# Performance work log

Hardware: AMD Instinct MI355X
Metric: run time of the kernel (lower is better)

The kernel has to match this reference:

```python
import jax, jax.numpy as jnp
import numpy as np

B, T, C, H = 2, 2048, 1024, 16
HD = C // H  # head dim = 64


def setup_inputs() -> dict:
    key = jax.random.key(0)
    k1, k2, k3 = jax.random.split(key, 3)
    scale = 0.02
    x = jax.random.normal(k1, (B, T, C), dtype=jnp.float32)
    w_attn = jax.random.normal(k2, (C, 3 * C), dtype=jnp.float32) * scale
    b_attn = jnp.zeros((3 * C,), dtype=jnp.float32)
    w_proj = jax.random.normal(k3, (C, C), dtype=jnp.float32) * scale
    b_proj = jnp.zeros((C,), dtype=jnp.float32)
    return {"x": x, "w_attn": w_attn, "b_attn": b_attn, "w_proj": w_proj, "b_proj": b_proj}


def reference(x, w_attn, b_attn, w_proj, b_proj):
    b, t, c = x.shape
    qkv = x @ w_attn + b_attn  # [B,T,3C]
    q, k, v = jnp.split(qkv, 3, axis=-1)
    # [B,T,C] -> [B,H,T,HD]
    q = q.reshape(b, t, H, HD).transpose(0, 2, 1, 3)
    k = k.reshape(b, t, H, HD).transpose(0, 2, 1, 3)
    v = v.reshape(b, t, H, HD).transpose(0, 2, 1, 3)
    att = jnp.einsum('bhqd,bhkd->bhqk', q, k) * (1.0 / jnp.sqrt(jnp.float32(HD)))
    causal = jnp.tril(jnp.ones((t, t), dtype=bool))  # [T,T]
    att = jnp.where(causal[None, None, :, :], att, jnp.float32(-jnp.inf))
    att = jax.nn.softmax(att, axis=-1)
    y = jnp.einsum('bhqk,bhkd->bhqd', att, v)
    y = y.transpose(0, 2, 1, 3).reshape(b, t, c)
    return y @ w_proj + b_proj
```

## Files before the change

kernel.cpp:

```cpp
#include <hip/hip_runtime.h>


typedef unsigned short u16;
typedef unsigned short u16x8 __attribute__((ext_vector_type(8)));
typedef unsigned short u16x4 __attribute__((ext_vector_type(4)));
typedef __bf16 bf16x8 __attribute__((ext_vector_type(8)));
typedef __bf16 bf16x4 __attribute__((ext_vector_type(4)));
typedef float f32x4 __attribute__((ext_vector_type(4)));

#define MFMA16(a, b, c) __builtin_amdgcn_mfma_f32_16x16x32_bf16(a, b, c, 0, 0, 0)

static __device__ __forceinline__ u16 f2b(float f) {
  union { float f; unsigned int i; } x; x.f = f;
  unsigned int r = x.i + 0x7fffu + ((x.i >> 16) & 1u);
  return (u16)(r >> 16);
}
static __device__ __forceinline__ float b2f(u16 u) {
  union { unsigned int i; float f; } x; x.i = ((unsigned int)u) << 16; return x.f;
}

static __device__ __forceinline__ void gload_lds16(const u16* g, u16* l) {
#if defined(__HIP_DEVICE_COMPILE__)
  __builtin_amdgcn_global_load_lds(
      (const __attribute__((address_space(1))) unsigned int*)g,
      (__attribute__((address_space(3))) unsigned int*)l,
      16, 0, 0);
#else
  (void)g; (void)l;
#endif
}

__global__ __launch_bounds__(256) void cast_f32_bf16(
    const float* __restrict__ in, u16* __restrict__ out) {
  int i = (blockIdx.x * 256 + threadIdx.x) * 8;
  float4 a = *(const float4*)&in[i];
  float4 b = *(const float4*)&in[i + 4];
  u16x8 o;
  o[0] = f2b(a.x); o[1] = f2b(a.y); o[2] = f2b(a.z); o[3] = f2b(a.w);
  o[4] = f2b(b.x); o[5] = f2b(b.y); o[6] = f2b(b.z); o[7] = f2b(b.w);
  *(u16x8*)&out[i] = o;
}

__global__ __launch_bounds__(256) void transpose_f32_bf16(
    const float* __restrict__ in, u16* __restrict__ out, int R, int Cc) {
  __shared__ u16 tile[32][33];
  int bx = blockIdx.x, by = blockIdx.y;
  int tx = threadIdx.x, ty = threadIdx.y;
#pragma unroll
  for (int i = 0; i < 4; i++) {
    int r = by * 32 + ty + i * 8;
    int c = bx * 32 + tx;
    tile[ty + i * 8][tx] = f2b(in[r * Cc + c]);
  }
  __syncthreads();
#pragma unroll
  for (int i = 0; i < 4; i++) {
    int r = bx * 32 + ty + i * 8;
    int c = by * 32 + tx;
    out[r * R + c] = tile[tx][ty + i * 8];
  }
}

template <int MODE>
__global__ __launch_bounds__(256, 3) void gemm_bt(
    const u16* __restrict__ A, const u16* __restrict__ Bt,
    const float* __restrict__ bias, float* __restrict__ out,
    u16* __restrict__ Qb, u16* __restrict__ Kb, u16* __restrict__ Vtb,
    int M, int N, int K) {
  __shared__ u16 lA[128 * 32];
  __shared__ u16 lB[128 * 32];

  const int tid = threadIdx.x;
  const int lane = tid & 63;
  const int w = tid >> 6;
  const int wm = (w >> 1) * 64, wn = (w & 1) * 64;
  const int l15 = lane & 15, quad = lane >> 4;

  const int nx = gridDim.x;
  const int id = blockIdx.y * nx + blockIdx.x;
  const int chunk = (nx * gridDim.y) >> 3;
  const int nid = (id & 7) * chunk + (id >> 3);
  const int m0 = (nid / nx) * 128, n0 = (nid % nx) * 128;

  const bool swapcd = (MODE == 0) && (n0 < 2048);

  const int srow = lane >> 2;
  const int scol = (lane & 3) * 8;

  f32x4 acc[4][4] = {};

  for (int k0 = 0; k0 < K; k0 += 32) {
    __syncthreads();
#pragma unroll
    for (int h = 0; h < 2; h++) {
      int r = h * 64 + w * 16 + srow;
      gload_lds16(&A[(m0 + r) * K + k0 + scol], &lA[h * 2048 + w * 512 + lane * 8]);
      gload_lds16(&Bt[(n0 + r) * K + k0 + scol], &lB[h * 2048 + w * 512 + lane * 8]);
    }
    __syncthreads();

    bf16x8 af[4], bfr[4];
#pragma unroll
    for (int mi = 0; mi < 4; mi++)
      af[mi] = *(const bf16x8*)&lA[(wm + mi * 16 + l15) * 32 + quad * 8];
#pragma unroll
    for (int ni = 0; ni < 4; ni++)
      bfr[ni] = *(const bf16x8*)&lB[(wn + ni * 16 + l15) * 32 + quad * 8];
    if (swapcd) {
#pragma unroll
      for (int mi = 0; mi < 4; mi++)
#pragma unroll
        for (int ni = 0; ni < 4; ni++)
          acc[mi][ni] = MFMA16(bfr[ni], af[mi], acc[mi][ni]);
    } else {
#pragma unroll
      for (int mi = 0; mi < 4; mi++)
#pragma unroll
        for (int ni = 0; ni < 4; ni++)
          acc[mi][ni] = MFMA16(af[mi], bfr[ni], acc[mi][ni]);
    }
  }

  if (MODE == 1) {
#pragma unroll
    for (int mi = 0; mi < 4; mi++) {
#pragma unroll
      for (int ni = 0; ni < 4; ni++) {
        int n = n0 + wn + ni * 16 + l15;
        float bv = bias[n];
#pragma unroll
        for (int reg = 0; reg < 4; reg++) {
          int m = m0 + wm + mi * 16 + quad * 4 + reg;
          out[m * N + n] = acc[mi][ni][reg] + bv;
        }
      }
    }
  } else if (n0 < 2048) {
    const int which = n0 >> 10;
    u16* dst = which ? Kb : Qb;
    const float scale = which ? 0.18033688011112042f : 1.0f;
    const int b = m0 >> 11;
    const int hh = ((n0 & 1023) + wn) >> 6;
    const int tbase = (m0 & 2047) + wm + l15;
#pragma unroll
    for (int mi = 0; mi < 4; mi++) {
      u16* drow = dst + (((b << 4) + hh) * 2048 + tbase + mi * 16) * 64;
#pragma unroll
      for (int ni = 0; ni < 4; ni++) {
        int d0 = ni * 16 + quad * 4;
        float4 bv4 = *(const float4*)&bias[n0 + wn + d0];
        u16x4 o;
        o[0] = f2b((acc[mi][ni][0] + bv4.x) * scale);
        o[1] = f2b((acc[mi][ni][1] + bv4.y) * scale);
        o[2] = f2b((acc[mi][ni][2] + bv4.z) * scale);
        o[3] = f2b((acc[mi][ni][3] + bv4.w) * scale);
        *(u16x4*)&drow[d0] = o;
      }
    }
  } else {
    const int b = m0 >> 11;
    const int hh = ((n0 & 1023) + wn) >> 6;
    const int bh = (b << 4) + hh;
    const u16* unused = A; (void)unused;
#pragma unroll
    for (int mi = 0; mi < 4; mi++) {
      int t32 = (m0 & 2047) + wm + (mi >> 1) * 32;
      int tp0 = quad * 8 + (mi & 1) * 4;
#pragma unroll
      for (int ni = 0; ni < 4; ni++) {
        int d = ni * 16 + l15;
        float bv = bias[n0 + wn + d];
        u16x4 o;
        o[0] = f2b(acc[mi][ni][0] + bv);
        o[1] = f2b(acc[mi][ni][1] + bv);
        o[2] = f2b(acc[mi][ni][2] + bv);
        o[3] = f2b(acc[mi][ni][3] + bv);
        *(u16x4*)&Vtb[(bh * 64 + d) * 2048 + t32 + tp0] = o;
      }
    }
  }
}

__global__ __launch_bounds__(256, 4) void attn_split(
    const u16* __restrict__ Qg, const u16* __restrict__ Kg,
    const u16* __restrict__ Vt, u16* __restrict__ Yg,
    u16* __restrict__ Opart, float* __restrict__ lpart) {
  __shared__ u16 lk[2][64 * 64];
  __shared__ u16 lvt[2][64 * 64];

  const int x = blockIdx.x;
  const int bh = blockIdx.y;
  int qt, s, ns;
  if (x < 8)       { qt = x;                s = 0;            ns = 1; }
  else if (x < 24) { int r = x - 8;  qt = 8  + (r >> 1); s = r & 1; ns = 2; }
  else if (x < 48) { int r = x - 24; qt = 16 + r / 3;    s = r % 3; ns = 3; }
  else             { int r = x - 48; qt = 24 + (r >> 2); s = r & 3; ns = 4; }
  const int total = qt + 1;
  const int kts  = (s * total) / ns;
  const int kend = ((s + 1) * total) / ns;

  const int tid = threadIdx.x;
  const int lane = tid & 63;
  const int w = tid >> 6;
  const int l15 = lane & 15, quad = lane >> 4;
  const int qbase = qt * 64;
  const int base = bh * 2048 * 64;
  const int vbase = bh * 64 * 2048;
  const int qloc = w * 16 + l15;
  const int xsw = (l15 & 7) << 3;

  const int sr = tid >> 3;
  const int sc = (tid & 7) * 8;

  const u16* qrow = Qg + base + (qbase + w * 16 + l15) * 64;
  bf16x8 bq0 = *(const bf16x8*)&qrow[quad * 8];
  bf16x8 bq1 = *(const bf16x8*)&qrow[32 + quad * 8];

  u16x8 onesu = {0x3F80, 0x3F80, 0x3F80, 0x3F80, 0x3F80, 0x3F80, 0x3F80, 0x3F80};
  bf16x8 ones = *(const bf16x8*)&onesu;

  const u16* kp = Kg + base;
  const u16* vp = Vt + vbase;

  u16x8 kr[2], vr[2];
  {
    int kvb = kts * 64;
#pragma unroll
    for (int h = 0; h < 2; h++) {
      int r = sr + h * 32;
      kr[h] = *(const u16x8*)&kp[(kvb + r) * 64 + sc];
      vr[h] = *(const u16x8*)&vp[r * 2048 + kvb + sc];
    }
  }

  f32x4 oacc[4] = {};
  f32x4 lacc = {};

  int cur = 0;
  for (int kt = kts; kt < kend; kt++) {
    u16* lkc = lk[cur];
    u16* lvc = lvt[cur];
#pragma unroll
    for (int h = 0; h < 2; h++) {
      int r = sr + h * 32;
      int cs = sc ^ ((r & 7) << 3);
      *(u16x8*)&lkc[r * 64 + cs] = kr[h];
      *(u16x8*)&lvc[r * 64 + cs] = vr[h];
    }
    __syncthreads();
    if (kt + 1 < kend) {
      int kvb = (kt + 1) * 64;
#pragma unroll
      for (int h = 0; h < 2; h++) {
        int r = sr + h * 32;
        kr[h] = *(const u16x8*)&kp[(kvb + r) * 64 + sc];
        vr[h] = *(const u16x8*)&vp[r * 2048 + kvb + sc];
      }
    }

    const bool diag = (kt == qt);

#pragma unroll
    for (int u = 0; u < 2; u++) {
      bf16x8 pa;
#pragma unroll
      for (int half = 0; half < 2; half++) {
        int nt = 2 * u + half;
        const u16* kb = &lkc[(nt * 16 + l15) * 64];
        bf16x8 ak0 = *(const bf16x8*)&kb[(quad * 8) ^ xsw];
        bf16x8 ak1 = *(const bf16x8*)&kb[(32 + quad * 8) ^ xsw];
        f32x4 st = {};
        st = MFMA16(ak0, bq0, st);
        st = MFMA16(ak1, bq1, st);
#pragma unroll
        for (int reg = 0; reg < 4; reg++) {
          float sv = st[reg];
          if (diag && (nt * 16 + quad * 4 + reg) > qloc) sv = -1e30f;
          pa[half * 4 + reg] = (__bf16)__builtin_amdgcn_exp2f(sv);
        }
      }
      lacc = MFMA16(pa, ones, lacc);
#pragma unroll
      for (int dt = 0; dt < 4; dt++) {
        bf16x8 bv = *(const bf16x8*)&lvc[(dt * 16 + l15) * 64 +
                                         ((u * 32 + quad * 8) ^ xsw)];
        oacc[dt] = MFMA16(pa, bv, oacc[dt]);
      }
    }
    cur ^= 1;
  }

  if (ns == 1) {
    const int b = bh >> 4, hh = bh & 15;
    float inv[4];
#pragma unroll
    for (int reg = 0; reg < 4; reg++) inv[reg] = 1.0f / lacc[reg];
#pragma unroll
    for (int dt = 0; dt < 4; dt++)
#pragma unroll
      for (int reg = 0; reg < 4; reg++) {
        int q = qbase + w * 16 + quad * 4 + reg;
        int col = hh * 64 + dt * 16 + l15;
        Yg[(b * 2048 + q) * 1024 + col] = f2b(oacc[dt][reg] * inv[reg]);
      }
  } else {
    const int p = bh * 80 + x;
    u16* op = Opart + p * 4096 + (w * 16) * 64;
#pragma unroll
    for (int dt = 0; dt < 4; dt++)
#pragma unroll
      for (int reg = 0; reg < 4; reg++)
        op[(quad * 4 + reg) * 64 + dt * 16 + l15] = f2b(oacc[dt][reg]);
    if (l15 == 0) {
#pragma unroll
      for (int reg = 0; reg < 4; reg++)
        lpart[p * 64 + w * 16 + quad * 4 + reg] = lacc[reg];
    }
  }
}

__global__ __launch_bounds__(256) void attn_combine(
    const u16* __restrict__ Opart, const float* __restrict__ lpart,
    u16* __restrict__ Yg) {
  const int qt = 8 + blockIdx.x;
  const int bh = blockIdx.y;
  const int tid = threadIdx.x;
  const int row = tid >> 2;
  const int cg = (tid & 3) * 16;
  int xb, ns;
  if (qt < 16)      { xb = 8  + (qt - 8) * 2;  ns = 2; }
  else if (qt < 24) { xb = 24 + (qt - 16) * 3; ns = 3; }
  else              { xb = 48 + (qt - 24) * 4; ns = 4; }

  float acc[16] = {};
  float lsum = 0.f;
  for (int i = 0; i < ns; i++) {
    int p = bh * 80 + xb + i;
    lsum += lpart[p * 64 + row];
    const u16* oprow = Opart + p * 4096 + row * 64 + cg;
    u16x8 a = *(const u16x8*)&oprow[0];
    u16x8 b = *(const u16x8*)&oprow[8];
#pragma unroll
    for (int j = 0; j < 8; j++) { acc[j] += b2f(a[j]); acc[8 + j] += b2f(b[j]); }
  }
  float inv = 1.0f / lsum;
  u16x8 o0, o1;
#pragma unroll
  for (int j = 0; j < 8; j++) { o0[j] = f2b(acc[j] * inv); o1[j] = f2b(acc[8 + j] * inv); }
  const int b = bh >> 4, hh = bh & 15;
  u16* y = Yg + ((long)(b * 2048 + qt * 64 + row)) * 1024 + hh * 64 + cg;
  *(u16x8*)&y[0] = o0;
  *(u16x8*)&y[8] = o1;
}

__global__ __launch_bounds__(256, 4) void attn_kernel(
    const u16* __restrict__ Qg, const u16* __restrict__ Kg,
    const u16* __restrict__ Vt, u16* __restrict__ Yg) {
  __shared__ u16 lk[64 * 64];
  __shared__ u16 lvt[64 * 64];

  const int qt = 31 - blockIdx.x;
  const int bh = blockIdx.y;
  const int tid = threadIdx.x;
  const int lane = tid & 63;
  const int w = tid >> 6;
  const int l15 = lane & 15, quad = lane >> 4;
  const int qbase = qt * 64;
  const int base = bh * 2048 * 64;
  const int vbase = bh * 64 * 2048;
  const int sr = tid >> 3;
  const int sc = (tid & 7) * 8;
  const int xsw = (l15 & 7) << 3;

  const u16* qrow = Qg + base + (qbase + w * 16 + l15) * 64;
  bf16x8 bq0 = *(const bf16x8*)&qrow[quad * 8];
  bf16x8 bq1 = *(const bf16x8*)&qrow[32 + quad * 8];

  u16x8 onesu = {0x3F80, 0x3F80, 0x3F80, 0x3F80, 0x3F80, 0x3F80, 0x3F80, 0x3F80};
  bf16x8 ones = *(const bf16x8*)&onesu;

  const u16* kp = Kg + base;
  const u16* vp = Vt + vbase;

  u16x8 kr[2], vr[2];
#pragma unroll
  for (int h = 0; h < 2; h++) {
    int r = sr + h * 32;
    kr[h] = *(const u16x8*)&kp[r * 64 + sc];
    vr[h] = *(const u16x8*)&vp[r * 2048 + sc];
  }

  f32x4 oacc[4] = {};
  f32x4 lacc = {};

  for (int kt = 0; kt <= qt; kt++) {
    __syncthreads();
#pragma unroll
    for (int h = 0; h < 2; h++) {
      int r = sr + h * 32;
      int cs = sc ^ ((r & 7) << 3);
      *(u16x8*)&lk[r * 64 + cs] = kr[h];
      *(u16x8*)&lvt[r * 64 + cs] = vr[h];
    }
    __syncthreads();
    if (kt < qt) {
      int kvb = (kt + 1) * 64;
#pragma unroll
      for (int h = 0; h < 2; h++) {
        int r = sr + h * 32;
        kr[h] = *(const u16x8*)&kp[(kvb + r) * 64 + sc];
        vr[h] = *(const u16x8*)&vp[r * 2048 + kvb + sc];
      }
    }

    const bool diag = (kt == qt);
    const int qloc = w * 16 + l15;
#pragma unroll
    for (int u = 0; u < 2; u++) {
      bf16x8 pa;
#pragma unroll
      for (int half = 0; half < 2; half++) {
        int nt = 2 * u + half;
        const u16* kb = &lk[(nt * 16 + l15) * 64];
        bf16x8 ak0 = *(const bf16x8*)&kb[(quad * 8) ^ xsw];
        bf16x8 ak1 = *(const bf16x8*)&kb[(32 + quad * 8) ^ xsw];
        f32x4 st = {};
        st = MFMA16(ak0, bq0, st);
        st = MFMA16(ak1, bq1, st);
#pragma unroll
        for (int reg = 0; reg < 4; reg++) {
          float sv = st[reg];
          if (diag && (nt * 16 + quad * 4 + reg) > qloc) sv = -1e30f;
          pa[half * 4 + reg] = (__bf16)__builtin_amdgcn_exp2f(sv);
        }
      }
      lacc = MFMA16(pa, ones, lacc);
#pragma unroll
      for (int dt = 0; dt < 4; dt++) {
        bf16x8 bv = *(const bf16x8*)&lvt[(dt * 16 + l15) * 64 +
                                         ((u * 32 + quad * 8) ^ xsw)];
        oacc[dt] = MFMA16(pa, bv, oacc[dt]);
      }
    }
  }

  const int b = bh >> 4, hh = bh & 15;
  float inv[4];
#pragma unroll
  for (int reg = 0; reg < 4; reg++) inv[reg] = 1.0f / lacc[reg];
#pragma unroll
  for (int dt = 0; dt < 4; dt++)
#pragma unroll
    for (int reg = 0; reg < 4; reg++) {
      int q = qbase + w * 16 + quad * 4 + reg;
      int col = hh * 64 + dt * 16 + l15;
      Yg[(b * 2048 + q) * 1024 + col] = f2b(oacc[dt][reg] * inv[reg]);
    }
}

extern "C" void kernel_launch(void* const* d_in, const int* in_sizes, int n_in,
                              void* d_out, int out_size, void* d_ws, size_t ws_size,
                              hipStream_t stream) {
  const float* x      = (const float*)d_in[0];
  const float* w_attn = (const float*)d_in[1];
  const float* b_attn = (const float*)d_in[2];
  const float* w_proj = (const float*)d_in[3];
  const float* b_proj = (const float*)d_in[4];
  float* out = (float*)d_out;

  char* ws = (char*)d_ws;
  u16* wattnT = (u16*)(ws);
  u16* wprojT = (u16*)(ws + 6291456);
  u16* xb     = (u16*)(ws + 8388608);
  u16* Qb     = (u16*)(ws + 16777216);
  u16* Kb     = (u16*)(ws + 25165824);
  u16* Vt     = (u16*)(ws + 33554432);
  u16* Yb     = (u16*)(ws + 41943040);
  u16* Opart  = (u16*)(ws + 50331648);
  float* lpart = (float*)(ws + 71303168);

  const bool split = (ws_size >= 71958528ULL);

  cast_f32_bf16<<<2048, 256, 0, stream>>>(x, xb);
  transpose_f32_bf16<<<dim3(96, 32), dim3(32, 8), 0, stream>>>(w_attn, wattnT, 1024, 3072);
  transpose_f32_bf16<<<dim3(32, 32), dim3(32, 8), 0, stream>>>(w_proj, wprojT, 1024, 1024);
  gemm_bt<0><<<dim3(24, 32), 256, 0, stream>>>(xb, wattnT, b_attn, nullptr,
                                               Qb, Kb, Vt, 4096, 3072, 1024);
  if (split) {
    attn_split<<<dim3(80, 32), 256, 0, stream>>>(Qb, Kb, Vt, Yb, Opart, lpart);
    attn_combine<<<dim3(24, 32), 256, 0, stream>>>(Opart, lpart, Yb);
  } else {
    attn_kernel<<<dim3(32, 32), 256, 0, stream>>>(Qb, Kb, Vt, Yb);
  }
  gemm_bt<1><<<dim3(8, 32), 256, 0, stream>>>(Yb, wprojT, b_proj, out,
                                              nullptr, nullptr, nullptr, 4096, 1024, 1024);
}
```

Baseline: 193.4 us.

## Merge prep kernels into one launch, raise attn occupancy, add MFMA priority

Folds the x cast and both weight transposes into a single prep kernel indexed by block id, so two kernel launches go away. Raises the attn_split launch bound from 4 to 5 blocks per CU and wraps the MFMA compute section in s_setprio to favour matrix issue. Also deletes the non-split attention fallback, so the split path now always runs whatever the workspace size. This risks register spills under the tighter occupancy bound and out-of-bounds writes if the workspace is ever too small for the partial buffers.

Measured after the change: 187.7 us. 1.03x faster.

```diff
diff --git a/kernel.cpp b/kernel.cpp
--- a/kernel.cpp
+++ b/kernel.cpp
@@ -30,22 +30,38 @@
 #endif
 }
 
-__global__ __launch_bounds__(256) void cast_f32_bf16(
-    const float* __restrict__ in, u16* __restrict__ out) {
-  int i = (blockIdx.x * 256 + threadIdx.x) * 8;
-  float4 a = *(const float4*)&in[i];
-  float4 b = *(const float4*)&in[i + 4];
-  u16x8 o;
-  o[0] = f2b(a.x); o[1] = f2b(a.y); o[2] = f2b(a.z); o[3] = f2b(a.w);
-  o[4] = f2b(b.x); o[5] = f2b(b.y); o[6] = f2b(b.z); o[7] = f2b(b.w);
-  *(u16x8*)&out[i] = o;
-}
-
-__global__ __launch_bounds__(256) void transpose_f32_bf16(
-    const float* __restrict__ in, u16* __restrict__ out, int R, int Cc) {
+__global__ __launch_bounds__(256) void prep(
+    const float* __restrict__ x, const float* __restrict__ w_attn,
+    const float* __restrict__ w_proj, u16* __restrict__ xb,
+    u16* __restrict__ wattnT, u16* __restrict__ wprojT) {
   __shared__ u16 tile[32][33];
-  int bx = blockIdx.x, by = blockIdx.y;
-  int tx = threadIdx.x, ty = threadIdx.y;
+  const int bid = blockIdx.x;
+  const int tid = threadIdx.x;
+
+  if (bid < 2048) {
+    int i = (bid * 256 + tid) * 8;
+    float4 a = *(const float4*)&x[i];
+    float4 b = *(const float4*)&x[i + 4];
+    u16x8 o;
+    o[0] = f2b(a.x); o[1] = f2b(a.y); o[2] = f2b(a.z); o[3] = f2b(a.w);
+    o[4] = f2b(b.x); o[5] = f2b(b.y); o[6] = f2b(b.z); o[7] = f2b(b.w);
+    *(u16x8*)&xb[i] = o;
+    return;
+  }
+
+  const float* in;
+  u16* out;
+  int bx, by, R, Cc;
+  if (bid < 5120) {
+    int b = bid - 2048;
+    bx = b % 96; by = b / 96; R = 1024; Cc = 3072;
+    in = w_attn; out = wattnT;
+  } else {
+    int b = bid - 5120;
+    bx = b % 32; by = b / 32; R = 1024; Cc = 1024;
+    in = w_proj; out = wprojT;
+  }
+  const int tx = tid & 31, ty = tid >> 5;
 #pragma unroll
   for (int i = 0; i < 4; i++) {
     int r = by * 32 + ty + i * 8;
@@ -161,7 +177,6 @@
     const int b = m0 >> 11;
     const int hh = ((n0 & 1023) + wn) >> 6;
     const int bh = (b << 4) + hh;
-    const u16* unused = A; (void)unused;
 #pragma unroll
     for (int mi = 0; mi < 4; mi++) {
       int t32 = (m0 & 2047) + wm + (mi >> 1) * 32;
@@ -181,7 +196,7 @@
   }
 }
 
-__global__ __launch_bounds__(256, 4) void attn_split(
+__global__ __launch_bounds__(256, 5) void attn_split(
     const u16* __restrict__ Qg, const u16* __restrict__ Kg,
     const u16* __restrict__ Vt, u16* __restrict__ Yg,
     u16* __restrict__ Opart, float* __restrict__ lpart) {
@@ -263,6 +278,7 @@
 #pragma unroll
     for (int u = 0; u < 2; u++) {
       bf16x8 pa;
+      __builtin_amdgcn_s_setprio(1);
 #pragma unroll
       for (int half = 0; half < 2; half++) {
         int nt = 2 * u + half;
@@ -286,6 +302,7 @@
                                          ((u * 32 + quad * 8) ^ xsw)];
         oacc[dt] = MFMA16(pa, bv, oacc[dt]);
       }
+      __builtin_amdgcn_s_setprio(0);
     }
     cur ^= 1;
   }
@@ -353,111 +370,6 @@
   *(u16x8*)&y[8] = o1;
 }
 
-__global__ __launch_bounds__(256, 4) void attn_kernel(
-    const u16* __restrict__ Qg, const u16* __restrict__ Kg,
-    const u16* __restrict__ Vt, u16* __restrict__ Yg) {
-  __shared__ u16 lk[64 * 64];
-  __shared__ u16 lvt[64 * 64];
-
-  const int qt = 31 - blockIdx.x;
-  const int bh = blockIdx.y;
-  const int tid = threadIdx.x;
-  const int lane = tid & 63;
-  const int w = tid >> 6;
-  const int l15 = lane & 15, quad = lane >> 4;
-  const int qbase = qt * 64;
-  const int base = bh * 2048 * 64;
-  const int vbase = bh * 64 * 2048;
-  const int sr = tid >> 3;
-  const int sc = (tid & 7) * 8;
-  const int xsw = (l15 & 7) << 3;
-
-  const u16* qrow = Qg + base + (qbase + w * 16 + l15) * 64;
-  bf16x8 bq0 = *(const bf16x8*)&qrow[quad * 8];
-  bf16x8 bq1 = *(const bf16x8*)&qrow[32 + quad * 8];
-
-  u16x8 onesu = {0x3F80, 0x3F80, 0x3F80, 0x3F80, 0x3F80, 0x3F80, 0x3F80, 0x3F80};
-  bf16x8 ones = *(const bf16x8*)&onesu;
-
-  const u16* kp = Kg + base;
-  const u16* vp = Vt + vbase;
-
-  u16x8 kr[2], vr[2];
-#pragma unroll
-  for (int h = 0; h < 2; h++) {
-    int r = sr + h * 32;
-    kr[h] = *(const u16x8*)&kp[r * 64 + sc];
-    vr[h] = *(const u16x8*)&vp[r * 2048 + sc];
-  }
-
-  f32x4 oacc[4] = {};
-  f32x4 lacc = {};
-
-  for (int kt = 0; kt <= qt; kt++) {
-    __syncthreads();
-#pragma unroll
-    for (int h = 0; h < 2; h++) {
-      int r = sr + h * 32;
-      int cs = sc ^ ((r & 7) << 3);
-      *(u16x8*)&lk[r * 64 + cs] = kr[h];
-      *(u16x8*)&lvt[r * 64 + cs] = vr[h];
-    }
-    __syncthreads();
-    if (kt < qt) {
-      int kvb = (kt + 1) * 64;
-#pragma unroll
-      for (int h = 0; h < 2; h++) {
-        int r = sr + h * 32;
-        kr[h] = *(const u16x8*)&kp[(kvb + r) * 64 + sc];
-        vr[h] = *(const u16x8*)&vp[r * 2048 + kvb + sc];
-      }
-    }
-
-    const bool diag = (kt == qt);
-    const int qloc = w * 16 + l15;
-#pragma unroll
-    for (int u = 0; u < 2; u++) {
-      bf16x8 pa;
-#pragma unroll
-      for (int half = 0; half < 2; half++) {
-        int nt = 2 * u + half;
-        const u16* kb = &lk[(nt * 16 + l15) * 64];
-        bf16x8 ak0 = *(const bf16x8*)&kb[(quad * 8) ^ xsw];
-        bf16x8 ak1 = *(const bf16x8*)&kb[(32 + quad * 8) ^ xsw];
-        f32x4 st = {};
-        st = MFMA16(ak0, bq0, st);
-        st = MFMA16(ak1, bq1, st);
-#pragma unroll
-        for (int reg = 0; reg < 4; reg++) {
-          float sv = st[reg];
-          if (diag && (nt * 16 + quad * 4 + reg) > qloc) sv = -1e30f;
-          pa[half * 4 + reg] = (__bf16)__builtin_amdgcn_exp2f(sv);
-        }
-      }
-      lacc = MFMA16(pa, ones, lacc);
-#pragma unroll
-      for (int dt = 0; dt < 4; dt++) {
-        bf16x8 bv = *(const bf16x8*)&lvt[(dt * 16 + l15) * 64 +
-                                         ((u * 32 + quad * 8) ^ xsw)];
-        oacc[dt] = MFMA16(pa, bv, oacc[dt]);
-      }
-    }
-  }
-
-  const int b = bh >> 4, hh = bh & 15;
-  float inv[4];
-#pragma unroll
-  for (int reg = 0; reg < 4; reg++) inv[reg] = 1.0f / lacc[reg];
-#pragma unroll
-  for (int dt = 0; dt < 4; dt++)
-#pragma unroll
-    for (int reg = 0; reg < 4; reg++) {
-      int q = qbase + w * 16 + quad * 4 + reg;
-      int col = hh * 64 + dt * 16 + l15;
-      Yg[(b * 2048 + q) * 1024 + col] = f2b(oacc[dt][reg] * inv[reg]);
-    }
-}
-
 extern "C" void kernel_launch(void* const* d_in, const int* in_sizes, int n_in,
                               void* d_out, int out_size, void* d_ws, size_t ws_size,
                               hipStream_t stream) {
@@ -479,19 +391,11 @@
   u16* Opart  = (u16*)(ws + 50331648);
   float* lpart = (float*)(ws + 71303168);
 
-  const bool split = (ws_size >= 71958528ULL);
-
-  cast_f32_bf16<<<2048, 256, 0, stream>>>(x, xb);
-  transpose_f32_bf16<<<dim3(96, 32), dim3(32, 8), 0, stream>>>(w_attn, wattnT, 1024, 3072);
-  transpose_f32_bf16<<<dim3(32, 32), dim3(32, 8), 0, stream>>>(w_proj, wprojT, 1024, 1024);
+  prep<<<6144, 256, 0, stream>>>(x, w_attn, w_proj, xb, wattnT, wprojT);
   gemm_bt<0><<<dim3(24, 32), 256, 0, stream>>>(xb, wattnT, b_attn, nullptr,
                                                Qb, Kb, Vt, 4096, 3072, 1024);
-  if (split) {
-    attn_split<<<dim3(80, 32), 256, 0, stream>>>(Qb, Kb, Vt, Yb, Opart, lpart);
-    attn_combine<<<dim3(24, 32), 256, 0, stream>>>(Opart, lpart, Yb);
-  } else {
-    attn_kernel<<<dim3(32, 32), 256, 0, stream>>>(Qb, Kb, Vt, Yb);
-  }
+  attn_split<<<dim3(80, 32), 256, 0, stream>>>(Qb, Kb, Vt, Yb, Opart, lpart);
+  attn_combine<<<dim3(24, 32), 256, 0, stream>>>(Opart, lpart, Yb);
   gemm_bt<1><<<dim3(8, 32), 256, 0, stream>>>(Yb, wprojT, b_proj, out,
                                               nullptr, nullptr, nullptr, 4096, 1024, 1024);
 }
```
